# Performance work log

Measured on AMD Instinct MI355X. Metric: run time of the kernel, lower is better.

Reference implementation:

```python
import jax, jax.numpy as jnp
import numpy as np

B, N, DIM = 1, 512, 1024
HEADS, DH = 16, 64          # dim_head = 64, _dim = heads*dh = 1024
P = 32                      # projection_dim
P2 = P // 2
NEG_INF = -1e30


def setup_inputs() -> dict:
    key = jax.random.key(0)
    ks = jax.random.split(key, 14)
    s = 0.02
    _dim = HEADS * DH
    return {
        "x":    jax.random.normal(ks[0], (B, N, DIM), dtype=jnp.float32),
        "Wqkv": jax.random.normal(ks[1], (3 * _dim, DIM), dtype=jnp.float32) * s,
        "Wout": jax.random.normal(ks[2], (DIM, _dim), dtype=jnp.float32) * s,
        "Wq":   jax.random.normal(ks[3], (P, DH), dtype=jnp.float32) * s,
        "bq":   jax.random.normal(ks[4], (P,), dtype=jnp.float32) * s,
        "Wk":   jax.random.normal(ks[5], (P, DH), dtype=jnp.float32) * s,
        "bk":   jax.random.normal(ks[6], (P,), dtype=jnp.float32) * s,
        "W1":   jax.random.normal(ks[7], (P, 2 * P), dtype=jnp.float32) * s,
        "b1":   jax.random.normal(ks[8], (P,), dtype=jnp.float32) * s,
        "W2":   jax.random.normal(ks[9], (P2, P), dtype=jnp.float32) * s,
        "b2":   jax.random.normal(ks[10], (P2,), dtype=jnp.float32) * s,
        "W3":   jax.random.normal(ks[11], (1, P2), dtype=jnp.float32) * s,
        "b3":   jax.random.normal(ks[12], (1,), dtype=jnp.float32) * s,
    }


def reference(x, Wqkv, Wout, Wq, bq, Wk, bk, W1, b1, W2, b2, W3, b3):
    b, n, _ = x.shape
    # qkv projection, then einops 'b n (d k h) -> k b h n d' split (d outermost!)
    qkv = jnp.einsum('bnc,oc->bno', x, Wqkv).reshape(b, n, DH, 3, HEADS)
    q = jnp.transpose(qkv[:, :, :, 0, :], (0, 3, 1, 2))  # [b,h,n,dh]
    k = jnp.transpose(qkv[:, :, :, 1, :], (0, 3, 1, 2))
    v = jnp.transpose(qkv[:, :, :, 2, :], (0, 3, 1, 2))

    qp = jnp.einsum('bhnd,pd->bhnp', q, Wq) + bq  # [b,h,n,P]
    kp = jnp.einsum('bhnd,pd->bhnp', k, Wk) + bk

    # linear1 on concat(q_i, k_j): split W1 -> broadcast-add (same math,
    # avoids materializing the [b,h,n,n,2P] concat tensor)
    W1q, W1k = W1[:, :P], W1[:, P:]
    a = jnp.einsum('bhnp,qp->bhnq', qp, W1q)      # [b,h,n,P]
    c = jnp.einsum('bhnp,qp->bhnq', kp, W1k)      # [b,h,n,P]
    h1 = jax.nn.relu(a[:, :, :, None, :] + c[:, :, None, :, :] + b1)  # [b,h,n,n,P]
    h2 = jax.nn.relu(jnp.einsum('bhijp,qp->bhijq', h1, W2) + b2)      # [b,h,n,n,P/2]
    score = jnp.einsum('bhijq,oq->bhijo', h2, W3)[..., 0] + b3[0]     # [b,h,n,n]

    # causal mask (triu(1) filled with -inf)
    i = jnp.arange(n)
    causal = i[None, :] > i[:, None]
    score = jnp.where(causal, NEG_INF, score)

    attn = jax.nn.softmax(score, axis=-1)
    out = jnp.einsum('bhij,bhjd->bhid', attn, v)                      # [b,h,n,dh]
    out = jnp.transpose(out, (0, 2, 1, 3)).reshape(b, n, HEADS * DH)  # b n (h d)
    return jnp.einsum('bne,oe->bno', out, Wout)
```

## Files before the change

### kernel.cpp

```cpp
#include <hip/hip_runtime.h>
#include <hip/hip_bf16.h>
#include <hip/hip_fp16.h>
#include <math.h>

#define N_SEQ 512
#define DIM   1024
#define HEADS 16
#define DH    64
#define P     32
#define P2    16
#define PSTR  520

typedef short    bf16x8 __attribute__((ext_vector_type(8)));
typedef _Float16 f16x8  __attribute__((ext_vector_type(8)));
typedef float    f32x4  __attribute__((ext_vector_type(4)));

__device__ inline unsigned short f2bf(float f) {
  union { float f; unsigned u; } v; v.f = f;
  unsigned r = (v.u + 0x7fffu + ((v.u >> 16) & 1u)) >> 16;
  return (unsigned short)r;
}

union H8 { f16x8 v; __half2 h2[4]; unsigned u32[4]; };

__global__ __launch_bounds__(256) void prep(
    const float* __restrict__ Wqkv, const float* __restrict__ Wq,
    const float* __restrict__ bq, const float* __restrict__ Wk,
    const float* __restrict__ bk, const float* __restrict__ W1,
    const float* __restrict__ x, const float* __restrict__ Wout,
    short* __restrict__ Wcomb, short* __restrict__ xb,
    short* __restrict__ Woutb, float* __restrict__ ba32,
    float* __restrict__ bc32) {
  const int b = blockIdx.x, tid = threadIdx.x;
  if (b < 256) {
    __shared__ float W1s[32][33];
    __shared__ float Wqs[32][65];
    __shared__ float wsm[32][65];
    __shared__ __align__(16) float qs[64][132];
    const int part = b >> 7, rem = b & 127;
    const int h = rem >> 3, c0 = (rem & 7) * 128;
    const int grow = part * 16 + h;
    for (int idx = tid; idx < 1024; idx += 256)
      W1s[idx >> 5][idx & 31] = W1[(idx >> 5) * 64 + part * 32 + (idx & 31)];
    const float* Wsel = part ? Wk : Wq;
    for (int idx = tid; idx < 2048; idx += 256)
      Wqs[idx >> 6][idx & 63] = Wsel[idx];
    for (int idx = tid; idx < 2048; idx += 256) {
      const int d = idx >> 5, c4 = idx & 31;
      *(float4*)&qs[d][c4 * 4] =
          *(const float4*)(Wqkv + (size_t)(d * 48 + grow) * DIM + c0 + c4 * 4);
    }
    __syncthreads();
    for (int idx = tid; idx < 2048; idx += 256) {
      const int q = idx >> 6, d = idx & 63;
      float s = 0.f;
#pragma unroll
      for (int p = 0; p < 32; ++p) s += W1s[q][p] * Wqs[p][d];
      wsm[q][d] = s;
    }
    __syncthreads();
    for (int idx = tid; idx < 4096; idx += 256) {
      const int q = idx >> 7, c = idx & 127;
      float s = 0.f;
#pragma unroll
      for (int d = 0; d < 64; ++d) s += wsm[q][d] * qs[d][c];
      Wcomb[(size_t)(part * 512 + h * 32 + q) * DIM + c0 + c] = (short)f2bf(s);
    }
    if (rem == 0 && tid < 32) {
      const float* bsel = part ? bk : bq;
      float s = 0.f;
#pragma unroll
      for (int p = 0; p < 32; ++p) s += W1s[tid][p] * bsel[p];
      (part ? bc32 : ba32)[tid] = s;
    }
  } else if (b < 384) {
#pragma unroll
    for (int rr = 0; rr < 8; ++rr) {
      const int ov = (b - 256) * 8 + rr;
      const int h = ov >> 6, d = ov & 63;
      const float4 v = *(const float4*)(Wqkv + (size_t)(d * 48 + 32 + h) * DIM + tid * 4);
      ushort4 o;
      o.x = f2bf(v.x); o.y = f2bf(v.y); o.z = f2bf(v.z); o.w = f2bf(v.w);
      *(ushort4*)(Wcomb + (size_t)(1024 + ov) * DIM + tid * 4) = o;
    }
  } else if (b < 512) {
    const int idx = (b - 384) * 256 + tid;
#pragma unroll
    for (int u = 0; u < 4; ++u) {
      const int t = u * 32768 + idx;
      const float4 v = ((const float4*)x)[t];
      ushort4 o;
      o.x = f2bf(v.x); o.y = f2bf(v.y); o.z = f2bf(v.z); o.w = f2bf(v.w);
      ((ushort4*)xb)[t] = o;
    }
  } else {
    const int idx = (b - 512) * 256 + tid;
#pragma unroll
    for (int u = 0; u < 4; ++u) {
      const int t = u * 65536 + idx;
      const float4 v = ((const float4*)Wout)[t];
      ushort4 o;
      o.x = f2bf(v.x); o.y = f2bf(v.y); o.z = f2bf(v.z); o.w = f2bf(v.w);
      ((ushort4*)Woutb)[t] = o;
    }
  }
}

__global__ __launch_bounds__(256) void gemm_acv(
    const short* __restrict__ xb, const short* __restrict__ Wcomb,
    const float* __restrict__ ba32, const float* __restrict__ bc32,
    const float* __restrict__ b1,
    __half* __restrict__ a_buf, __half* __restrict__ cb_buf,
    __half* __restrict__ vT) {
  const int wave = blockIdx.x * 4 + (threadIdx.x >> 6);
  const int tm = wave >> 6;
  const int tn = wave & 63;
  const int lane = threadIdx.x & 63;
  const int m = lane & 15;
  const int quad = lane >> 4;

  const short* pa  = xb + (size_t)(tm * 16 + m) * DIM + quad * 8;
  const short* pb0 = Wcomb + (size_t)(tn * 32 + m) * DIM + quad * 8;
  const short* pb1 = pb0 + (size_t)16 * DIM;

  f32x4 acc0 = {0.f,0.f,0.f,0.f}, acc1 = {0.f,0.f,0.f,0.f};
#pragma unroll 4
  for (int k = 0; k < DIM; k += 32) {
    const bf16x8 av = *(const bf16x8*)(pa + k);
    const bf16x8 b0 = *(const bf16x8*)(pb0 + k);
    const bf16x8 b1v = *(const bf16x8*)(pb1 + k);
    acc0 = __builtin_amdgcn_mfma_f32_16x16x32_bf16(av, b0, acc0, 0, 0, 0);
    acc1 = __builtin_amdgcn_mfma_f32_16x16x32_bf16(av, b1v, acc1, 0, 0, 0);
  }

#pragma unroll
  for (int r = 0; r < 4; ++r) {
    const int n = tm * 16 + quad * 4 + r;
#pragma unroll
    for (int half = 0; half < 2; ++half) {
      const int o = tn * 32 + m + half * 16;
      const float val = half ? acc1[r] : acc0[r];
      if (o < 512) {
        const int h = o >> 5, q = o & 31;
        a_buf[((size_t)h * N_SEQ + n) * P + q] = __float2half(val + ba32[q]);
      } else if (o < 1024) {
        const int oo = o - 512, h = oo >> 5, q = oo & 31;
        cb_buf[((size_t)h * N_SEQ + n) * P + q] = __float2half(val + bc32[q] + b1[q]);
      } else {
        const int ov = o - 1024, h = ov >> 6, d = ov & 63;
        vT[((size_t)h * DH + d) * N_SEQ + n] = __float2half(val);
      }
    }
  }
}

__device__ inline float rowscore(const H8& a, const H8& c, f16x8 w2f,
                                 float4 b2q, float4 w3q) {
  H8 u;
#pragma unroll
  for (int k = 0; k < 4; ++k) {
    const __half2 s = __hadd2(a.h2[k], c.h2[k]);
    union { __half2 h; unsigned u; } cv; cv.h = s;
    const unsigned msk = (cv.u >> 15) & 0x00010001u;
    u.u32[k] = cv.u & ~(msk * 0xFFFFu);
  }
  f32x4 acc = {0.f, 0.f, 0.f, 0.f};
  acc = __builtin_amdgcn_mfma_f32_16x16x32_f16(w2f, u.v, acc, 0, 0, 0);
  return fmaxf(acc[0] + b2q.x, 0.f) * w3q.x + fmaxf(acc[1] + b2q.y, 0.f) * w3q.y
       + fmaxf(acc[2] + b2q.z, 0.f) * w3q.z + fmaxf(acc[3] + b2q.w, 0.f) * w3q.w;
}

__device__ inline float quadreduce4(float p0, float p1, float p2, float p3,
                                    int quad) {
  const float sx = (quad & 1) ? p0 : p1;
  const float sy = (quad & 1) ? p2 : p3;
  const float rx = __shfl_xor(sx, 16);
  const float ry = __shfl_xor(sy, 16);
  const float aa = ((quad & 1) ? p1 : p0) + rx;
  const float bb = ((quad & 1) ? p3 : p2) + ry;
  const float sz = (quad & 2) ? aa : bb;
  const float rz = __shfl_xor(sz, 32);
  return ((quad & 2) ? bb : aa) + rz;
}

__global__ __launch_bounds__(256) void attn_fused(
    const __half* __restrict__ a_g, const __half* __restrict__ cb_g,
    const float* __restrict__ W2, const float* __restrict__ b2,
    const float* __restrict__ W3,
    const __half* __restrict__ vT, short* __restrict__ attnb) {
  const int p = blockIdx.x;
  const int h = blockIdx.y;
  const int tid = threadIdx.x;
  const int w = tid >> 6;
  const int lane = tid & 63;
  const int m = lane & 15, quad = lane >> 4;

  __shared__ __align__(16) __half probS[32][PSTR];
  __shared__ float invS[32];

  const int tlo = p, thi = 31 - p;
  const int nlo = p + 1, nhi = 32 - p;

  {
    f16x8 w2f;
    {
      const float4* wp = (const float4*)(W2 + m * P + quad * 8);
      const float4 w0 = wp[0], w1 = wp[1];
      H8 u;
      u.h2[0] = __floats2half2_rn(w0.x, w0.y);
      u.h2[1] = __floats2half2_rn(w0.z, w0.w);
      u.h2[2] = __floats2half2_rn(w1.x, w1.y);
      u.h2[3] = __floats2half2_rn(w1.z, w1.w);
      w2f = u.v;
    }
    const float4 b2q = *(const float4*)(b2 + quad * 4);
    const float4 w3q = *(const float4*)(W3 + quad * 4);

    H8 alo[4], ahi[4];
#pragma unroll
    for (int r = 0; r < 4; ++r) {
      alo[r].v = *(const f16x8*)(a_g + ((size_t)h * N_SEQ + tlo * 16 + 4 * w + r) * P + quad * 8);
      ahi[r].v = *(const f16x8*)(a_g + ((size_t)h * N_SEQ + thi * 16 + 4 * w + r) * P + quad * 8);
    }

    for (int jt = 0; jt < nhi; ++jt) {
      H8 cb;
      cb.v = *(const f16x8*)(cb_g + ((size_t)h * N_SEQ + jt * 16 + m) * P + quad * 8);
      const float q0 = rowscore(ahi[0], cb, w2f, b2q, w3q);
      const float q1 = rowscore(ahi[1], cb, w2f, b2q, w3q);
      const float q2 = rowscore(ahi[2], cb, w2f, b2q, w3q);
      const float q3 = rowscore(ahi[3], cb, w2f, b2q, w3q);
      const float fh = quadreduce4(q0, q1, q2, q3, quad);
      probS[16 + 4 * w + quad][jt * 16 + m] = __float2half(fh);
      if (jt < nlo) {
        const float s0 = rowscore(alo[0], cb, w2f, b2q, w3q);
        const float s1 = rowscore(alo[1], cb, w2f, b2q, w3q);
        const float s2 = rowscore(alo[2], cb, w2f, b2q, w3q);
        const float s3 = rowscore(alo[3], cb, w2f, b2q, w3q);
        const float fl = quadreduce4(s0, s1, s2, s3, quad);
        probS[4 * w + quad][jt * 16 + m] = __float2half(fl);
      }
    }
  }
  __syncthreads();

  {
    const int lr = 8 * w + (lane >> 3);
    const int c  = lane & 7;
    const int gi = (lr < 16) ? (tlo * 16 + lr) : (thi * 16 + (lr - 16));
    float mx = -1e30f;
#pragma unroll
    for (int k = 0; k < 8; ++k) {
      const int c0 = k * 64 + c * 8;
      if (c0 > gi) break;
      H8 vv; vv.v = *(const f16x8*)&probS[lr][c0];
#pragma unroll
      for (int u = 0; u < 8; ++u) {
        const float s = __half2float(vv.h2[u >> 1].data[u & 1]);
        if (c0 + u <= gi) mx = fmaxf(mx, s);
      }
    }
#pragma unroll
    for (int msk = 1; msk < 8; msk <<= 1) mx = fmaxf(mx, __shfl_xor(mx, msk));
    float sum = 0.f;
#pragma unroll
    for (int k = 0; k < 8; ++k) {
      const int c0 = k * 64 + c * 8;
      H8 vv; vv.v = *(const f16x8*)&probS[lr][c0];
      H8 o;
#pragma unroll
      for (int u = 0; u < 4; ++u) {
        float e0 = 0.f, e1 = 0.f;
        if (c0 + 2 * u <= gi) {
          e0 = __expf(__half2float(vv.h2[u].data[0]) - mx);
          if (c0 + 2 * u + 1 <= gi)
            e1 = __expf(__half2float(vv.h2[u].data[1]) - mx);
        }
        sum += e0 + e1;
        o.h2[u] = __floats2half2_rn(e0, e1);
      }
      *(f16x8*)&probS[lr][c0] = o.v;
    }
#pragma unroll
    for (int msk = 1; msk < 8; msk <<= 1) sum += __shfl_xor(sum, msk);
    if (c == 0) invS[lr] = 1.f / sum;
  }
  __syncthreads();

  {
    const int d0 = w * 16;
    const __half* pb = vT + ((size_t)h * DH + d0 + m) * N_SEQ + quad * 8;
#pragma unroll
    for (int half = 0; half < 2; ++half) {
      const int lbase = half ? 16 : 0;
      const int tile = half ? thi : tlo;
      const int nk = half ? ((33 - p) >> 1) : ((p + 2) >> 1);
      f32x4 acc = {0.f, 0.f, 0.f, 0.f};
      for (int k = 0; k < nk; ++k) {
        const f16x8 a = *(const f16x8*)&probS[lbase + m][k * 32 + quad * 8];
        const f16x8 b = *(const f16x8*)(pb + k * 32);
        acc = __builtin_amdgcn_mfma_f32_16x16x32_f16(a, b, acc, 0, 0, 0);
      }
#pragma unroll
      for (int r = 0; r < 4; ++r) {
        const int lrow = quad * 4 + r;
        const float val = acc[r] * invS[lbase + lrow];
        attnb[(size_t)(tile * 16 + lrow) * DIM + h * DH + d0 + m] = (short)f2bf(val);
      }
    }
  }
}

__global__ __launch_bounds__(256) void gemm_out16(
    const short* __restrict__ A, const short* __restrict__ B,
    float* __restrict__ C) {
  const int wave = blockIdx.x * 4 + (threadIdx.x >> 6);
  const int tm = wave >> 6;
  const int tn = wave & 63;
  const int lane = threadIdx.x & 63;
  const int m = lane & 15, quad = lane >> 4;

  const short* pa = A + (size_t)(tm * 16 + m) * DIM + quad * 8;
  const short* pb = B + (size_t)(tn * 16 + m) * DIM + quad * 8;

  f32x4 acc = {0.f, 0.f, 0.f, 0.f};
#pragma unroll 4
  for (int k = 0; k < DIM; k += 32) {
    const bf16x8 a = *(const bf16x8*)(pa + k);
    const bf16x8 b = *(const bf16x8*)(pb + k);
    acc = __builtin_amdgcn_mfma_f32_16x16x32_bf16(a, b, acc, 0, 0, 0);
  }
#pragma unroll
  for (int r = 0; r < 4; ++r)
    C[(size_t)(tm * 16 + quad * 4 + r) * DIM + tn * 16 + m] = acc[r];
}

extern "C" void kernel_launch(void* const* d_in, const int* in_sizes, int n_in,
                              void* d_out, int out_size, void* d_ws, size_t ws_size,
                              hipStream_t stream) {
  const float* x    = (const float*)d_in[0];
  const float* Wqkv = (const float*)d_in[1];
  const float* Wout = (const float*)d_in[2];
  const float* Wq   = (const float*)d_in[3];
  const float* bq   = (const float*)d_in[4];
  const float* Wk   = (const float*)d_in[5];
  const float* bk   = (const float*)d_in[6];
  const float* W1   = (const float*)d_in[7];
  const float* b1   = (const float*)d_in[8];
  const float* W2   = (const float*)d_in[9];
  const float* b2   = (const float*)d_in[10];
  const float* W3   = (const float*)d_in[11];
  float* out = (float*)d_out;

  float*  ws     = (float*)d_ws;
  float*  ba32   = ws;
  float*  bc32   = ba32 + 32;
  __half* a_buf  = (__half*)(bc32 + 32);
  __half* cb_buf = a_buf + (size_t)HEADS * N_SEQ * P;
  __half* vT     = cb_buf + (size_t)HEADS * N_SEQ * P;
  short*  Wcomb  = (short*)(vT + (size_t)HEADS * DH * N_SEQ);
  short*  xb     = Wcomb + (size_t)2048 * DIM;
  short*  Woutb  = xb + (size_t)N_SEQ * DIM;
  short*  attnb  = Woutb + (size_t)DIM * DIM;

  prep<<<768, 256, 0, stream>>>(Wqkv, Wq, bq, Wk, bk, W1, x, Wout,
                                Wcomb, xb, Woutb, ba32, bc32);

  gemm_acv<<<512, 256, 0, stream>>>(xb, Wcomb, ba32, bc32, b1,
                                    a_buf, cb_buf, vT);

  dim3 g3(16, HEADS);
  attn_fused<<<g3, 256, 0, stream>>>(a_buf, cb_buf, W2, b2, W3, vT, attnb);

  gemm_out16<<<512, 256, 0, stream>>>(attnb, Woutb, out);
}
```

Measured before the change: 174.8 us.

## Merge all four kernels into one cooperative persistent kernel with grid syncs

```diff
diff --git a/kernel.cpp b/kernel.cpp
--- a/kernel.cpp
+++ b/kernel.cpp
@@ -1,7 +1,10 @@
 #include <hip/hip_runtime.h>
 #include <hip/hip_bf16.h>
 #include <hip/hip_fp16.h>
+#include <hip/hip_cooperative_groups.h>
 #include <math.h>
+
+namespace cg = cooperative_groups;
 
 #define N_SEQ 512
 #define DIM   1024
@@ -23,20 +26,81 @@
 
 union H8 { f16x8 v; __half2 h2[4]; unsigned u32[4]; };
 
-__global__ __launch_bounds__(256) void prep(
-    const float* __restrict__ Wqkv, const float* __restrict__ Wq,
+union LdsU {
+  struct { float W1s[32][33]; float Wqs[32][65]; float wsm[32][65]; float qs[64][132]; } p0;
+  struct { unsigned short probS[32][PSTR]; float invS[32]; } p2;
+};
+
+__device__ inline float rowscore(const H8& a, const H8& c, f16x8 w2f,
+                                 f32x4 b2q, float4 w3q) {
+  const f16x8 z = (f16x8)(_Float16)0;
+  const f16x8 u = __builtin_elementwise_max(a.v + c.v, z);
+  f32x4 acc = b2q;
+  acc = __builtin_amdgcn_mfma_f32_16x16x32_f16(w2f, u, acc, 0, 0, 0);
+  return fmaxf(acc[0], 0.f) * w3q.x + fmaxf(acc[1], 0.f) * w3q.y
+       + fmaxf(acc[2], 0.f) * w3q.z + fmaxf(acc[3], 0.f) * w3q.w;
+}
+
+__device__ inline float quadreduce4(float p0, float p1, float p2, float p3,
+                                    int quad) {
+  const float sx = (quad & 1) ? p0 : p1;
+  const float sy = (quad & 1) ? p2 : p3;
+  const float rx = __shfl_xor(sx, 16);
+  const float ry = __shfl_xor(sy, 16);
+  const float aa = ((quad & 1) ? p1 : p0) + rx;
+  const float bb = ((quad & 1) ? p3 : p2) + ry;
+  const float sz = (quad & 2) ? aa : bb;
+  const float rz = __shfl_xor(sz, 32);
+  return ((quad & 2) ? bb : aa) + rz;
+}
+
+__global__ __launch_bounds__(256) void fused_all(
+    const float* __restrict__ x, const float* __restrict__ Wqkv,
+    const float* __restrict__ Wout, const float* __restrict__ Wq,
     const float* __restrict__ bq, const float* __restrict__ Wk,
     const float* __restrict__ bk, const float* __restrict__ W1,
-    const float* __restrict__ x, const float* __restrict__ Wout,
-    short* __restrict__ Wcomb, short* __restrict__ xb,
-    short* __restrict__ Woutb, float* __restrict__ ba32,
-    float* __restrict__ bc32) {
+    const float* __restrict__ b1, const float* __restrict__ W2,
+    const float* __restrict__ b2, const float* __restrict__ W3,
+    float* __restrict__ out,
+    float* __restrict__ ba32, float* __restrict__ bc32,
+    __half* __restrict__ a_buf, __half* __restrict__ cb_buf,
+    __half* __restrict__ vT, short* __restrict__ Wcomb,
+    short* __restrict__ xb, short* __restrict__ Woutb,
+    short* __restrict__ attnb) {
   const int b = blockIdx.x, tid = threadIdx.x;
-  if (b < 256) {
-    __shared__ float W1s[32][33];
-    __shared__ float Wqs[32][65];
-    __shared__ float wsm[32][65];
-    __shared__ __align__(16) float qs[64][132];
+  __shared__ __align__(16) LdsU sh;
+  cg::grid_group grid = cg::this_grid();
+
+  {
+#pragma unroll
+    for (int u = 0; u < 2; ++u) {
+      const int t = b * 512 + u * 256 + tid;
+      const float4 v = ((const float4*)x)[t];
+      ushort4 o;
+      o.x = f2bf(v.x); o.y = f2bf(v.y); o.z = f2bf(v.z); o.w = f2bf(v.w);
+      ((ushort4*)xb)[t] = o;
+    }
+#pragma unroll
+    for (int u = 0; u < 4; ++u) {
+      const int t = b * 1024 + u * 256 + tid;
+      const float4 v = ((const float4*)Wout)[t];
+      ushort4 o;
+      o.x = f2bf(v.x); o.y = f2bf(v.y); o.z = f2bf(v.z); o.w = f2bf(v.w);
+      ((ushort4*)Woutb)[t] = o;
+    }
+#pragma unroll
+    for (int rr = 0; rr < 4; ++rr) {
+      const int ov = b * 4 + rr;
+      const int hv = ov >> 6, dv = ov & 63;
+      const float4 v = *(const float4*)(Wqkv + (size_t)(dv * 48 + 32 + hv) * DIM + tid * 4);
+      ushort4 o;
+      o.x = f2bf(v.x); o.y = f2bf(v.y); o.z = f2bf(v.z); o.w = f2bf(v.w);
+      *(ushort4*)(Wcomb + (size_t)(1024 + ov) * DIM + tid * 4) = o;
+    }
+    float (*W1s)[33]  = sh.p0.W1s;
+    float (*Wqs)[65]  = sh.p0.Wqs;
+    float (*wsm)[65]  = sh.p0.wsm;
+    float (*qs)[132]  = sh.p0.qs;
     const int part = b >> 7, rem = b & 127;
     const int h = rem >> 3, c0 = (rem & 7) * 128;
     const int grow = part * 16 + h;
@@ -55,7 +119,7 @@
       const int q = idx >> 6, d = idx & 63;
       float s = 0.f;
 #pragma unroll
-      for (int p = 0; p < 32; ++p) s += W1s[q][p] * Wqs[p][d];
+      for (int pp = 0; pp < 32; ++pp) s += W1s[q][pp] * Wqs[pp][d];
       wsm[q][d] = s;
     }
     __syncthreads();
@@ -70,269 +134,203 @@
       const float* bsel = part ? bk : bq;
       float s = 0.f;
 #pragma unroll
-      for (int p = 0; p < 32; ++p) s += W1s[tid][p] * bsel[p];
+      for (int pp = 0; pp < 32; ++pp) s += W1s[tid][pp] * bsel[pp];
+      if (part) s += b1[tid];
       (part ? bc32 : ba32)[tid] = s;
     }
-  } else if (b < 384) {
-#pragma unroll
-    for (int rr = 0; rr < 8; ++rr) {
-      const int ov = (b - 256) * 8 + rr;
-      const int h = ov >> 6, d = ov & 63;
-      const float4 v = *(const float4*)(Wqkv + (size_t)(d * 48 + 32 + h) * DIM + tid * 4);
-      ushort4 o;
-      o.x = f2bf(v.x); o.y = f2bf(v.y); o.z = f2bf(v.z); o.w = f2bf(v.w);
-      *(ushort4*)(Wcomb + (size_t)(1024 + ov) * DIM + tid * 4) = o;
-    }
-  } else if (b < 512) {
-    const int idx = (b - 384) * 256 + tid;
-#pragma unroll
-    for (int u = 0; u < 4; ++u) {
-      const int t = u * 32768 + idx;
-      const float4 v = ((const float4*)x)[t];
-      ushort4 o;
-      o.x = f2bf(v.x); o.y = f2bf(v.y); o.z = f2bf(v.z); o.w = f2bf(v.w);
-      ((ushort4*)xb)[t] = o;
-    }
-  } else {
-    const int idx = (b - 512) * 256 + tid;
-#pragma unroll
-    for (int u = 0; u < 4; ++u) {
-      const int t = u * 65536 + idx;
-      const float4 v = ((const float4*)Wout)[t];
-      ushort4 o;
-      o.x = f2bf(v.x); o.y = f2bf(v.y); o.z = f2bf(v.z); o.w = f2bf(v.w);
-      ((ushort4*)Woutb)[t] = o;
-    }
   }
-}
-
-__global__ __launch_bounds__(256) void gemm_acv(
-    const short* __restrict__ xb, const short* __restrict__ Wcomb,
-    const float* __restrict__ ba32, const float* __restrict__ bc32,
-    const float* __restrict__ b1,
-    __half* __restrict__ a_buf, __half* __restrict__ cb_buf,
-    __half* __restrict__ vT) {
-  const int wave = blockIdx.x * 4 + (threadIdx.x >> 6);
-  const int tm = wave >> 6;
-  const int tn = wave & 63;
-  const int lane = threadIdx.x & 63;
-  const int m = lane & 15;
-  const int quad = lane >> 4;
-
-  const short* pa  = xb + (size_t)(tm * 16 + m) * DIM + quad * 8;
-  const short* pb0 = Wcomb + (size_t)(tn * 32 + m) * DIM + quad * 8;
-  const short* pb1 = pb0 + (size_t)16 * DIM;
-
-  f32x4 acc0 = {0.f,0.f,0.f,0.f}, acc1 = {0.f,0.f,0.f,0.f};
+  grid.sync();
+
+  {
+    const int lane = tid & 63;
+    const int m = lane & 15;
+    const int quad = lane >> 4;
+#pragma unroll
+    for (int u = 0; u < 2; ++u) {
+      const int wave = b * 4 + (tid >> 6) + u * 1024;
+      const int tm = wave >> 6;
+      const int tn = wave & 63;
+      const short* pa  = xb + (size_t)(tm * 16 + m) * DIM + quad * 8;
+      const short* pb0 = Wcomb + (size_t)(tn * 32 + m) * DIM + quad * 8;
+      const short* pb1 = pb0 + (size_t)16 * DIM;
+      f32x4 acc0 = {0.f,0.f,0.f,0.f}, acc1 = {0.f,0.f,0.f,0.f};
 #pragma unroll 4
-  for (int k = 0; k < DIM; k += 32) {
-    const bf16x8 av = *(const bf16x8*)(pa + k);
-    const bf16x8 b0 = *(const bf16x8*)(pb0 + k);
-    const bf16x8 b1v = *(const bf16x8*)(pb1 + k);
-    acc0 = __builtin_amdgcn_mfma_f32_16x16x32_bf16(av, b0, acc0, 0, 0, 0);
-    acc1 = __builtin_amdgcn_mfma_f32_16x16x32_bf16(av, b1v, acc1, 0, 0, 0);
+      for (int k = 0; k < DIM; k += 32) {
+        const bf16x8 av  = *(const bf16x8*)(pa + k);
+        const bf16x8 b0  = *(const bf16x8*)(pb0 + k);
+        const bf16x8 b1v = *(const bf16x8*)(pb1 + k);
+        acc0 = __builtin_amdgcn_mfma_f32_16x16x32_bf16(av, b0, acc0, 0, 0, 0);
+        acc1 = __builtin_amdgcn_mfma_f32_16x16x32_bf16(av, b1v, acc1, 0, 0, 0);
+      }
+#pragma unroll
+      for (int r = 0; r < 4; ++r) {
+        const int n = tm * 16 + quad * 4 + r;
+#pragma unroll
+        for (int half = 0; half < 2; ++half) {
+          const int o = tn * 32 + m + half * 16;
+          const float val = half ? acc1[r] : acc0[r];
+          if (o < 512) {
+            const int hh = o >> 5, q = o & 31;
+            a_buf[((size_t)hh * N_SEQ + n) * P + q] = __float2half(val + ba32[q]);
+          } else if (o < 1024) {
+            const int oo = o - 512, hh = oo >> 5, q = oo & 31;
+            cb_buf[((size_t)hh * N_SEQ + n) * P + q] = __float2half(val + bc32[q]);
+          } else {
+            const int ov = o - 1024, hh = ov >> 6, d = ov & 63;
+            vT[((size_t)hh * DH + d) * N_SEQ + n] = __float2half(val);
+          }
+        }
+      }
+    }
   }
-
-#pragma unroll
-  for (int r = 0; r < 4; ++r) {
-    const int n = tm * 16 + quad * 4 + r;
-#pragma unroll
-    for (int half = 0; half < 2; ++half) {
-      const int o = tn * 32 + m + half * 16;
-      const float val = half ? acc1[r] : acc0[r];
-      if (o < 512) {
-        const int h = o >> 5, q = o & 31;
-        a_buf[((size_t)h * N_SEQ + n) * P + q] = __float2half(val + ba32[q]);
-      } else if (o < 1024) {
-        const int oo = o - 512, h = oo >> 5, q = oo & 31;
-        cb_buf[((size_t)h * N_SEQ + n) * P + q] = __float2half(val + bc32[q] + b1[q]);
-      } else {
-        const int ov = o - 1024, h = ov >> 6, d = ov & 63;
-        vT[((size_t)h * DH + d) * N_SEQ + n] = __float2half(val);
+  grid.sync();
+
+  {
+    const int p = b & 15;
+    const int h = b >> 4;
+    const int w = tid >> 6;
+    const int lane = tid & 63;
+    const int m = lane & 15, quad = lane >> 4;
+    __half (*probS)[PSTR] = reinterpret_cast<__half(*)[PSTR]>(sh.p2.probS);
+    float* invS = sh.p2.invS;
+
+    const int tlo = p, thi = 31 - p;
+    const int nlo = p + 1, nhi = 32 - p;
+
+    {
+      f16x8 w2f;
+      {
+        const float4* wp = (const float4*)(W2 + m * P + quad * 8);
+        const float4 w0 = wp[0], w1 = wp[1];
+        H8 uu;
+        uu.h2[0] = __floats2half2_rn(w0.x, w0.y);
+        uu.h2[1] = __floats2half2_rn(w0.z, w0.w);
+        uu.h2[2] = __floats2half2_rn(w1.x, w1.y);
+        uu.h2[3] = __floats2half2_rn(w1.z, w1.w);
+        w2f = uu.v;
+      }
+      const float4 b2f = *(const float4*)(b2 + quad * 4);
+      const f32x4 b2q = {b2f.x, b2f.y, b2f.z, b2f.w};
+      const float4 w3q = *(const float4*)(W3 + quad * 4);
+
+      H8 alo[4], ahi[4];
+#pragma unroll
+      for (int r = 0; r < 4; ++r) {
+        alo[r].v = *(const f16x8*)(a_buf + ((size_t)h * N_SEQ + tlo * 16 + 4 * w + r) * P + quad * 8);
+        ahi[r].v = *(const f16x8*)(a_buf + ((size_t)h * N_SEQ + thi * 16 + 4 * w + r) * P + quad * 8);
+      }
+
+      for (int jt = 0; jt < nhi; ++jt) {
+        H8 cb;
+        cb.v = *(const f16x8*)(cb_buf + ((size_t)h * N_SEQ + jt * 16 + m) * P + quad * 8);
+        const float q0 = rowscore(ahi[0], cb, w2f, b2q, w3q);
+        const float q1 = rowscore(ahi[1], cb, w2f, b2q, w3q);
+        const float q2 = rowscore(ahi[2], cb, w2f, b2q, w3q);
+        const float q3 = rowscore(ahi[3], cb, w2f, b2q, w3q);
+        const float fh = quadreduce4(q0, q1, q2, q3, quad);
+        probS[16 + 4 * w + quad][jt * 16 + m] = __float2half(fh);
+        if (jt < nlo) {
+          const float s0 = rowscore(alo[0], cb, w2f, b2q, w3q);
+          const float s1 = rowscore(alo[1], cb, w2f, b2q, w3q);
+          const float s2 = rowscore(alo[2], cb, w2f, b2q, w3q);
+          const float s3 = rowscore(alo[3], cb, w2f, b2q, w3q);
+          const float fl = quadreduce4(s0, s1, s2, s3, quad);
+          probS[4 * w + quad][jt * 16 + m] = __float2half(fl);
+        }
+      }
+    }
+    __syncthreads();
+
+    {
+      const int lr = 8 * w + (lane >> 3);
+      const int c  = lane & 7;
+      const int gi = (lr < 16) ? (tlo * 16 + lr) : (thi * 16 + (lr - 16));
+      float mx = -1e30f;
+#pragma unroll
+      for (int k = 0; k < 8; ++k) {
+        const int c0 = k * 64 + c * 8;
+        if (c0 > gi) break;
+        H8 vv; vv.v = *(const f16x8*)&probS[lr][c0];
+#pragma unroll
+        for (int uu = 0; uu < 8; ++uu) {
+          const float s = __half2float(vv.h2[uu >> 1].data[uu & 1]);
+          if (c0 + uu <= gi) mx = fmaxf(mx, s);
+        }
+      }
+#pragma unroll
+      for (int msk = 1; msk < 8; msk <<= 1) mx = fmaxf(mx, __shfl_xor(mx, msk));
+      float sum = 0.f;
+#pragma unroll
+      for (int k = 0; k < 8; ++k) {
+        const int c0 = k * 64 + c * 8;
+        H8 vv; vv.v = *(const f16x8*)&probS[lr][c0];
+        H8 o;
+#pragma unroll
+        for (int uu = 0; uu < 4; ++uu) {
+          float e0 = 0.f, e1 = 0.f;
+          if (c0 + 2 * uu <= gi) {
+            e0 = __expf(__half2float(vv.h2[uu].data[0]) - mx);
+            if (c0 + 2 * uu + 1 <= gi)
+              e1 = __expf(__half2float(vv.h2[uu].data[1]) - mx);
+          }
+          sum += e0 + e1;
+          o.h2[uu] = __floats2half2_rn(e0, e1);
+        }
+        *(f16x8*)&probS[lr][c0] = o.v;
+      }
+#pragma unroll
+      for (int msk = 1; msk < 8; msk <<= 1) sum += __shfl_xor(sum, msk);
+      if (c == 0) invS[lr] = 1.f / sum;
+    }
+    __syncthreads();
+
+    {
+      const int d0 = w * 16;
+      const __half* pb = vT + ((size_t)h * DH + d0 + m) * N_SEQ + quad * 8;
+#pragma unroll
+      for (int half = 0; half < 2; ++half) {
+        const int lbase = half ? 16 : 0;
+        const int tile = half ? thi : tlo;
+        const int nk = half ? ((33 - p) >> 1) : ((p + 2) >> 1);
+        f32x4 acc = {0.f, 0.f, 0.f, 0.f};
+        for (int k = 0; k < nk; ++k) {
+          const f16x8 aa = *(const f16x8*)&probS[lbase + m][k * 32 + quad * 8];
+          const f16x8 bb = *(const f16x8*)(pb + k * 32);
+          acc = __builtin_amdgcn_mfma_f32_16x16x32_f16(aa, bb, acc, 0, 0, 0);
+        }
+#pragma unroll
+        for (int r = 0; r < 4; ++r) {
+          const int lrow = quad * 4 + r;
+          const float val = acc[r] * invS[lbase + lrow];
+          attnb[(size_t)(tile * 16 + lrow) * DIM + h * DH + d0 + m] = (short)f2bf(val);
+        }
       }
     }
   }
-}
-
-__device__ inline float rowscore(const H8& a, const H8& c, f16x8 w2f,
-                                 float4 b2q, float4 w3q) {
-  H8 u;
-#pragma unroll
-  for (int k = 0; k < 4; ++k) {
-    const __half2 s = __hadd2(a.h2[k], c.h2[k]);
-    union { __half2 h; unsigned u; } cv; cv.h = s;
-    const unsigned msk = (cv.u >> 15) & 0x00010001u;
-    u.u32[k] = cv.u & ~(msk * 0xFFFFu);
+  grid.sync();
+
+  {
+    const int lane = tid & 63;
+    const int m = lane & 15, quad = lane >> 4;
+#pragma unroll
+    for (int u = 0; u < 2; ++u) {
+      const int wave = b * 4 + (tid >> 6) + u * 1024;
+      const int tm = wave >> 6;
+      const int tn = wave & 63;
+      const short* pa = attnb + (size_t)(tm * 16 + m) * DIM + quad * 8;
+      const short* pb = Woutb + (size_t)(tn * 16 + m) * DIM + quad * 8;
+      f32x4 acc = {0.f, 0.f, 0.f, 0.f};
+#pragma unroll 4
+      for (int k = 0; k < DIM; k += 32) {
+        const bf16x8 aa = *(const bf16x8*)(pa + k);
+        const bf16x8 bb = *(const bf16x8*)(pb + k);
+        acc = __builtin_amdgcn_mfma_f32_16x16x32_bf16(aa, bb, acc, 0, 0, 0);
+      }
+#pragma unroll
+      for (int r = 0; r < 4; ++r)
+        out[(size_t)(tm * 16 + quad * 4 + r) * DIM + tn * 16 + m] = acc[r];
+    }
   }
-  f32x4 acc = {0.f, 0.f, 0.f, 0.f};
-  acc = __builtin_amdgcn_mfma_f32_16x16x32_f16(w2f, u.v, acc, 0, 0, 0);
-  return fmaxf(acc[0] + b2q.x, 0.f) * w3q.x + fmaxf(acc[1] + b2q.y, 0.f) * w3q.y
-       + fmaxf(acc[2] + b2q.z, 0.f) * w3q.z + fmaxf(acc[3] + b2q.w, 0.f) * w3q.w;
-}
-
-__device__ inline float quadreduce4(float p0, float p1, float p2, float p3,
-                                    int quad) {
-  const float sx = (quad & 1) ? p0 : p1;
-  const float sy = (quad & 1) ? p2 : p3;
-  const float rx = __shfl_xor(sx, 16);
-  const float ry = __shfl_xor(sy, 16);
-  const float aa = ((quad & 1) ? p1 : p0) + rx;
-  const float bb = ((quad & 1) ? p3 : p2) + ry;
-  const float sz = (quad & 2) ? aa : bb;
-  const float rz = __shfl_xor(sz, 32);
-  return ((quad & 2) ? bb : aa) + rz;
-}
-
-__global__ __launch_bounds__(256) void attn_fused(
-    const __half* __restrict__ a_g, const __half* __restrict__ cb_g,
-    const float* __restrict__ W2, const float* __restrict__ b2,
-    const float* __restrict__ W3,
-    const __half* __restrict__ vT, short* __restrict__ attnb) {
-  const int p = blockIdx.x;
-  const int h = blockIdx.y;
-  const int tid = threadIdx.x;
-  const int w = tid >> 6;
-  const int lane = tid & 63;
-  const int m = lane & 15, quad = lane >> 4;
-
-  __shared__ __align__(16) __half probS[32][PSTR];
-  __shared__ float invS[32];
-
-  const int tlo = p, thi = 31 - p;
-  const int nlo = p + 1, nhi = 32 - p;
-
-  {
-    f16x8 w2f;
-    {
-      const float4* wp = (const float4*)(W2 + m * P + quad * 8);
-      const float4 w0 = wp[0], w1 = wp[1];
-      H8 u;
-      u.h2[0] = __floats2half2_rn(w0.x, w0.y);
-      u.h2[1] = __floats2half2_rn(w0.z, w0.w);
-      u.h2[2] = __floats2half2_rn(w1.x, w1.y);
-      u.h2[3] = __floats2half2_rn(w1.z, w1.w);
-      w2f = u.v;
-    }
-    const float4 b2q = *(const float4*)(b2 + quad * 4);
-    const float4 w3q = *(const float4*)(W3 + quad * 4);
-
-    H8 alo[4], ahi[4];
-#pragma unroll
-    for (int r = 0; r < 4; ++r) {
-      alo[r].v = *(const f16x8*)(a_g + ((size_t)h * N_SEQ + tlo * 16 + 4 * w + r) * P + quad * 8);
-      ahi[r].v = *(const f16x8*)(a_g + ((size_t)h * N_SEQ + thi * 16 + 4 * w + r) * P + quad * 8);
-    }
-
-    for (int jt = 0; jt < nhi; ++jt) {
-      H8 cb;
-      cb.v = *(const f16x8*)(cb_g + ((size_t)h * N_SEQ + jt * 16 + m) * P + quad * 8);
-      const float q0 = rowscore(ahi[0], cb, w2f, b2q, w3q);
-      const float q1 = rowscore(ahi[1], cb, w2f, b2q, w3q);
-      const float q2 = rowscore(ahi[2], cb, w2f, b2q, w3q);
-      const float q3 = rowscore(ahi[3], cb, w2f, b2q, w3q);
-      const float fh = quadreduce4(q0, q1, q2, q3, quad);
-      probS[16 + 4 * w + quad][jt * 16 + m] = __float2half(fh);
-      if (jt < nlo) {
-        const float s0 = rowscore(alo[0], cb, w2f, b2q, w3q);
-        const float s1 = rowscore(alo[1], cb, w2f, b2q, w3q);
-        const float s2 = rowscore(alo[2], cb, w2f, b2q, w3q);
-        const float s3 = rowscore(alo[3], cb, w2f, b2q, w3q);
-        const float fl = quadreduce4(s0, s1, s2, s3, quad);
-        probS[4 * w + quad][jt * 16 + m] = __float2half(fl);
-      }
-    }
-  }
-  __syncthreads();
-
-  {
-    const int lr = 8 * w + (lane >> 3);
-    const int c  = lane & 7;
-    const int gi = (lr < 16) ? (tlo * 16 + lr) : (thi * 16 + (lr - 16));
-    float mx = -1e30f;
-#pragma unroll
-    for (int k = 0; k < 8; ++k) {
-      const int c0 = k * 64 + c * 8;
-      if (c0 > gi) break;
-      H8 vv; vv.v = *(const f16x8*)&probS[lr][c0];
-#pragma unroll
-      for (int u = 0; u < 8; ++u) {
-        const float s = __half2float(vv.h2[u >> 1].data[u & 1]);
-        if (c0 + u <= gi) mx = fmaxf(mx, s);
-      }
-    }
-#pragma unroll
-    for (int msk = 1; msk < 8; msk <<= 1) mx = fmaxf(mx, __shfl_xor(mx, msk));
-    float sum = 0.f;
-#pragma unroll
-    for (int k = 0; k < 8; ++k) {
-      const int c0 = k * 64 + c * 8;
-      H8 vv; vv.v = *(const f16x8*)&probS[lr][c0];
-      H8 o;
-#pragma unroll
-      for (int u = 0; u < 4; ++u) {
-        float e0 = 0.f, e1 = 0.f;
-        if (c0 + 2 * u <= gi) {
-          e0 = __expf(__half2float(vv.h2[u].data[0]) - mx);
-          if (c0 + 2 * u + 1 <= gi)
-            e1 = __expf(__half2float(vv.h2[u].data[1]) - mx);
-        }
-        sum += e0 + e1;
-        o.h2[u] = __floats2half2_rn(e0, e1);
-      }
-      *(f16x8*)&probS[lr][c0] = o.v;
-    }
-#pragma unroll
-    for (int msk = 1; msk < 8; msk <<= 1) sum += __shfl_xor(sum, msk);
-    if (c == 0) invS[lr] = 1.f / sum;
-  }
-  __syncthreads();
-
-  {
-    const int d0 = w * 16;
-    const __half* pb = vT + ((size_t)h * DH + d0 + m) * N_SEQ + quad * 8;
-#pragma unroll
-    for (int half = 0; half < 2; ++half) {
-      const int lbase = half ? 16 : 0;
-      const int tile = half ? thi : tlo;
-      const int nk = half ? ((33 - p) >> 1) : ((p + 2) >> 1);
-      f32x4 acc = {0.f, 0.f, 0.f, 0.f};
-      for (int k = 0; k < nk; ++k) {
-        const f16x8 a = *(const f16x8*)&probS[lbase + m][k * 32 + quad * 8];
-        const f16x8 b = *(const f16x8*)(pb + k * 32);
-        acc = __builtin_amdgcn_mfma_f32_16x16x32_f16(a, b, acc, 0, 0, 0);
-      }
-#pragma unroll
-      for (int r = 0; r < 4; ++r) {
-        const int lrow = quad * 4 + r;
-        const float val = acc[r] * invS[lbase + lrow];
-        attnb[(size_t)(tile * 16 + lrow) * DIM + h * DH + d0 + m] = (short)f2bf(val);
-      }
-    }
-  }
-}
-
-__global__ __launch_bounds__(256) void gemm_out16(
-    const short* __restrict__ A, const short* __restrict__ B,
-    float* __restrict__ C) {
-  const int wave = blockIdx.x * 4 + (threadIdx.x >> 6);
-  const int tm = wave >> 6;
-  const int tn = wave & 63;
-  const int lane = threadIdx.x & 63;
-  const int m = lane & 15, quad = lane >> 4;
-
-  const short* pa = A + (size_t)(tm * 16 + m) * DIM + quad * 8;
-  const short* pb = B + (size_t)(tn * 16 + m) * DIM + quad * 8;
-
-  f32x4 acc = {0.f, 0.f, 0.f, 0.f};
-#pragma unroll 4
-  for (int k = 0; k < DIM; k += 32) {
-    const bf16x8 a = *(const bf16x8*)(pa + k);
-    const bf16x8 b = *(const bf16x8*)(pb + k);
-    acc = __builtin_amdgcn_mfma_f32_16x16x32_bf16(a, b, acc, 0, 0, 0);
-  }
-#pragma unroll
-  for (int r = 0; r < 4; ++r)
-    C[(size_t)(tm * 16 + quad * 4 + r) * DIM + tn * 16 + m] = acc[r];
 }
 
 extern "C" void kernel_launch(void* const* d_in, const int* in_sizes, int n_in,
@@ -363,14 +361,13 @@
   short*  Woutb  = xb + (size_t)N_SEQ * DIM;
   short*  attnb  = Woutb + (size_t)DIM * DIM;
 
-  prep<<<768, 256, 0, stream>>>(Wqkv, Wq, bq, Wk, bk, W1, x, Wout,
-                                Wcomb, xb, Woutb, ba32, bc32);
-
-  gemm_acv<<<512, 256, 0, stream>>>(xb, Wcomb, ba32, bc32, b1,
-                                    a_buf, cb_buf, vT);
-
-  dim3 g3(16, HEADS);
-  attn_fused<<<g3, 256, 0, stream>>>(a_buf, cb_buf, W2, b2, W3, vT, attnb);
-
-  gemm_out16<<<512, 256, 0, stream>>>(attnb, Woutb, out);
-}
+  void* args[] = {
+      (void*)&x, (void*)&Wqkv, (void*)&Wout, (void*)&Wq, (void*)&bq,
+      (void*)&Wk, (void*)&bk, (void*)&W1, (void*)&b1, (void*)&W2,
+      (void*)&b2, (void*)&W3, (void*)&out, (void*)&ba32, (void*)&bc32,
+      (void*)&a_buf, (void*)&cb_buf, (void*)&vT, (void*)&Wcomb,
+      (void*)&xb, (void*)&Woutb, (void*)&attnb};
+
+  (void)hipLaunchCooperativeKernel(fused_all, dim3(256), dim3(256), args, 0,
+                                   stream);
+}
```

Result: slower. 271.3 us (+55.2%).
